# Performance work log

Measured on AMD Instinct MI355X. Metric: run time of the kernel, lower is better.

The kernel has to match this reference:

```python
import jax, jax.numpy as jnp
import numpy as np

N = 50000          # num nodes
DEG = 16           # fixed degree (uniform CSR)
E = N * DEG        # num edges
R = 8              # num relations
IN = 128
HID = 128
OUT = 40
BN_EPS = 1e-5


def setup_inputs() -> dict:
    key = jax.random.key(0)
    k = jax.random.split(key, 5)
    x = jax.random.normal(k[0], (N, IN), jnp.float32)
    # glorot-ish init for per-relation weights
    W1 = jax.random.normal(k[1], (R, IN, HID), jnp.float32) * (2.0 / (IN + HID)) ** 0.5
    W2 = jax.random.normal(k[2], (R, HID, OUT), jnp.float32) * (2.0 / (HID + OUT)) ** 0.5
    ptr = jnp.arange(N + 1, dtype=jnp.int32) * DEG            # CSR row offsets
    idx = jax.random.randint(k[3], (E,), 0, N, jnp.int32)     # neighbor (src) ids
    edge_types = jax.random.randint(k[4], (E,), 0, R, jnp.int32)
    return {
        "x": x, "W1": W1, "W2": W2,
        "bn_gamma": jnp.ones((HID,), jnp.float32),
        "bn_beta": jnp.zeros((HID,), jnp.float32),
        "bn_mean": jnp.zeros((HID,), jnp.float32),
        "bn_var": jnp.ones((HID,), jnp.float32),
        "ptr": ptr, "idx": idx, "edge_types": edge_types,
    }


def _rgcn_layer(h, W, ptr, idx, edge_types):
    # RGCNOP: out[i] = sum_{e in [ptr[i],ptr[i+1])} x[idx[e]] @ W[etype[e]]
    # Efficient form: transform every node by every relation once, then gather
    # the (src, etype) pair per edge and scatter-add into destinations.
    xr = jnp.einsum('nd,rdh->nrh', h, W)             # [N, R, H]
    msgs = xr[idx, edge_types]                       # [E, H] irregular gather
    deg = ptr[1:] - ptr[:-1]                         # [N]
    dst = jnp.repeat(jnp.arange(ptr.shape[0] - 1, dtype=jnp.int32), deg,
                     total_repeat_length=idx.shape[0])
    agg = jax.ops.segment_sum(msgs, dst, num_segments=ptr.shape[0] - 1)
    return agg / deg[:, None].astype(agg.dtype)      # degree normalization


def reference(x, W1, W2, bn_gamma, bn_beta, bn_mean, bn_var, ptr, idx, edge_types):
    h = _rgcn_layer(x, W1, ptr, idx, edge_types)
    # BatchNorm1d in eval mode (history_size=0, dropout inactive)
    h = (h - bn_mean) * jax.lax.rsqrt(bn_var + BN_EPS) * bn_gamma + bn_beta
    h = jax.nn.relu(h)
    h = _rgcn_layer(h, W2, ptr, idx, edge_types)
    return jax.nn.log_softmax(h, axis=-1)
```

## Files before the change

kernel.cpp:

```cpp
#include <hip/hip_runtime.h>
#include <math.h>

typedef __attribute__((ext_vector_type(8))) short bf16x8;
typedef __attribute__((ext_vector_type(4))) float f32x4;

constexpr int kN   = 50000;
constexpr int kIn  = 128;
constexpr int kHid = 128;
constexpr int kOut = 40;
constexpr int kNT  = 16;
constexpr int kLds = 1032;
constexpr float kBnEps = 1e-5f;

constexpr size_t kOffW2hi = 262144;
constexpr size_t kOffW2z  = 360448;
constexpr size_t kOffXb   = 524288;
constexpr size_t kOffBig  = 13324288;
constexpr size_t kZBytes  = (size_t)kN * 512 * 2;

__device__ inline float bf2f(ushort s) { return __uint_as_float(((uint)s) << 16); }

__device__ __forceinline__ ushort f2bf(float x) {
    uint u = __float_as_uint(x);
    u += 0x7FFFu + ((u >> 16) & 1u);
    return (ushort)(u >> 16);
}

__device__ __forceinline__ uint cvtpk(float a, float b) {
    uint r;
    asm("v_cvt_pk_bf16_f32 %0, %1, %2" : "=v"(r) : "v"(a), "v"(b));
    return r;
}

#define RD(V, J) __builtin_amdgcn_readlane((V), (J))

__device__ __forceinline__ void pack_unit(const float* __restrict__ W,
                                          ushort* __restrict__ dst,
                                          int N, int frag, int lane)
{
    const int kt = frag & 31;
    const int nt = frag >> 5;
    const int n  = nt * 16 + (lane & 15);
    const int q  = lane >> 4;
    float f[8];
    #pragma unroll
    for (int j = 0; j < 8; ++j) {
        const int k = kt * 32 + q * 8 + j;
        f[j] = (n < N) ? W[(size_t)k * N + n] : 0.f;
    }
    const size_t o = ((size_t)frag * 64 + lane) * 8;
    *(uint4*)&dst[o] = make_uint4(cvtpk(f[0], f[1]), cvtpk(f[2], f[3]),
                                  cvtpk(f[4], f[5]), cvtpk(f[6], f[7]));
}

__global__ __launch_bounds__(256)
void prep(const float* __restrict__ x,  ushort* __restrict__ xb,
          const float* __restrict__ W1, ushort* __restrict__ W1hi,
          const float* __restrict__ W2, ushort* __restrict__ W2hi,
          ushort* __restrict__ W2z, int useZ)
{
    const int b   = blockIdx.x;
    const int tid = threadIdx.x;
    if (b < 3125) {
        const size_t i = ((size_t)b * 256 + tid) * 8;
        const float4 v0 = *(const float4*)&x[i];
        const float4 v1 = *(const float4*)&x[i + 4];
        *(uint4*)&xb[i] = make_uint4(cvtpk(v0.x, v0.y), cvtpk(v0.z, v0.w),
                                     cvtpk(v1.x, v1.y), cvtpk(v1.z, v1.w));
    } else if (b < 3125 + 64) {
        pack_unit(W1, W1hi, kHid, (b - 3125) * 4 + (tid >> 6), tid & 63);
    } else if (b < 3213) {
        const int frag = (b - 3189) * 4 + (tid >> 6);
        if (frag < 96) pack_unit(W2, W2hi, kOut, frag, tid & 63);
    } else if (useZ) {
        const int frag = (b - 3213) * 4 + (tid >> 6);
        const int kt   = frag & 3;
        const int nt   = frag >> 2;
        const int lane = tid & 63;
        const int c    = nt * 16 + (lane & 15);
        const int r    = c >> 6;
        const int o    = c & 63;
        const int q    = lane >> 4;
        float f[8];
        #pragma unroll
        for (int j = 0; j < 8; ++j) {
            const int k = kt * 32 + q * 8 + j;
            f[j] = (o < kOut) ? W2[((size_t)r * kHid + k) * kOut + o] : 0.f;
        }
        const size_t of = ((size_t)frag * 64 + lane) * 8;
        *(uint4*)&W2z[of] = make_uint4(cvtpk(f[0], f[1]), cvtpk(f[2], f[3]),
                                       cvtpk(f[4], f[5]), cvtpk(f[6], f[7]));
    }
}

__device__ __forceinline__ void stage_fast(const char* fb, int vi, char* msW,
                                           int hOff, int lane)
{
    const int b = (lane & 7) * 16;
    #pragma unroll
    for (int u = 0; u < 4; ++u) {
        const int e   = u * 8 + (lane >> 3);
        const int src = __shfl(vi, e, 64);
        const uint4 v = *(const uint4*)(fb + (((size_t)(uint)src) << 8) + hOff + b);
        *(uint4*)(msW + e * 128 + (b ^ (u << 5))) = v;
    }
}

__device__ __forceinline__ void stage_slow(const char* fb,
                                           const int* __restrict__ idx,
                                           int p0, int p1, int deg0, int deg1,
                                           char* msW, int hOff, int lane)
{
    const int l31 = lane & 31;
    if (lane < 32) {
        for (int e = 0; e < 32; ++e) {
            const bool eok = (e < 16) ? (e < deg0) : ((e - 16) < deg1);
            uint val = 0;
            if (eok) {
                const int g = (e < 16) ? (p0 + e) : (p1 + (e - 16));
                const int s = idx[g];
                val = *(const uint*)(fb + (((size_t)(uint)s) << 8) + hOff + l31 * 4);
            }
            *(uint*)(msW + e * 128 + ((l31 * 4) ^ (((e >> 3) & 3) << 5))) = val;
        }
    }
}

__device__ __forceinline__ bf16x8 readB(const char* msW, int q, int m, int ntL)
{
    const char* ap = msW + q * 1024 + 2 * m + (((ntL ^ q) & 3) << 5);
    bf16x8 b;
    #pragma unroll
    for (int j = 0; j < 8; ++j) b[j] = *(const short*)(ap + j * 128);
    return b;
}

__device__ __forceinline__ void mfma_store(bf16x8 aS, bf16x8 bb, int fbase,
                                           int ntL, int w, int q, int m,
                                           ushort (*aggHi)[kLds])
{
    f32x4 z = {0.f, 0.f, 0.f, 0.f};
    const f32x4 d = __builtin_amdgcn_mfma_f32_16x16x32_bf16(aS, bb, z, 0, 0, 0);
    ushort* dst = &aggHi[2 * w + (q >> 1)][0];
    const int fcol = fbase + ntL * 16 + m;
    const int rb   = (q & 1) * 4;
    dst[(rb + 0) * 128 + fcol] = f2bf(d[0]);
    dst[(rb + 1) * 128 + fcol] = f2bf(d[1]);
    dst[(rb + 2) * 128 + fcol] = f2bf(d[2]);
    dst[(rb + 3) * 128 + fcol] = f2bf(d[3]);
}

__device__ __forceinline__ void phaseA_mfma(const ushort* __restrict__ feat,
                                            const int* __restrict__ ptr,
                                            const int* __restrict__ idx,
                                            const int* __restrict__ etype,
                                            int base, ushort (*aggHi)[kLds],
                                            char* msgs)
{
    const int lane = threadIdx.x & 63;
    const int w    = threadIdx.x >> 6;
    const int m    = lane & 15;
    const int q    = lane >> 4;
    const char* fb = (const char*)feat;

    const int node0 = base + 2 * w;
    const int p0 = ptr[node0];
    const int p1 = ptr[node0 + 1];
    const int p2 = ptr[node0 + 2];
    const int deg0 = p1 - p0, deg1 = p2 - p1;
    const bool fast = (deg0 == 16) && (deg1 == 16);

    const int vi = idx  [p0 + (lane & 31)];
    const int ve = etype[p0 + (lane & 31)];

    char* msW = msgs + w * 4096;

    int code;
    if (fast) {
        code = (((lane & 31) >> 4) << 3) | ve;
    } else {
        const int l31 = lane & 31;
        const bool eok = (l31 < 16) ? (l31 < deg0) : ((l31 - 16) < deg1);
        code = eok ? (((l31 >> 4) << 3) | ve) : 0xFF;
    }

    bf16x8 aS;
    #pragma unroll
    for (int j = 0; j < 8; ++j) {
        const int cj = __shfl(code, q * 8 + j, 64);
        aS[j] = (cj == m) ? (short)0x3F80 : (short)0;
    }

    if (fast) stage_fast(fb, vi, msW, 0, lane);
    else      stage_slow(fb, idx, p0, p1, deg0, deg1, msW, 0, lane);
    const bf16x8 b0 = readB(msW, q, m, 0);
    const bf16x8 b1 = readB(msW, q, m, 1);
    const bf16x8 b2 = readB(msW, q, m, 2);
    const bf16x8 b3 = readB(msW, q, m, 3);

    if (fast) stage_fast(fb, vi, msW, 128, lane);
    else      stage_slow(fb, idx, p0, p1, deg0, deg1, msW, 128, lane);

    mfma_store(aS, b0, 0, 0, w, q, m, aggHi);
    mfma_store(aS, b1, 0, 1, w, q, m, aggHi);
    mfma_store(aS, b2, 0, 2, w, q, m, aggHi);
    mfma_store(aS, b3, 0, 3, w, q, m, aggHi);

    const bf16x8 c0 = readB(msW, q, m, 0);
    const bf16x8 c1 = readB(msW, q, m, 1);
    const bf16x8 c2 = readB(msW, q, m, 2);
    const bf16x8 c3 = readB(msW, q, m, 3);
    mfma_store(aS, c0, 64, 0, w, q, m, aggHi);
    mfma_store(aS, c1, 64, 1, w, q, m, aggHi);
    mfma_store(aS, c2, 64, 2, w, q, m, aggHi);
    mfma_store(aS, c3, 64, 3, w, q, m, aggHi);
}

__global__ __launch_bounds__(512, 4)
void rgcn_layer1(const ushort* __restrict__ xb,
                 const ushort* __restrict__ W1hi,
                 const ushort* __restrict__ W2z,
                 const float* __restrict__ gamma, const float* __restrict__ beta,
                 const float* __restrict__ mean,  const float* __restrict__ var,
                 const int* __restrict__ ptr, const int* __restrict__ idx,
                 const int* __restrict__ etype,
                 ushort* __restrict__ big, int useZ)
{
    __shared__ ushort aggHi[kNT][kLds];
    __shared__ __align__(16) char msgs[8 * 4096];
    const int tid  = threadIdx.x;
    const int base = blockIdx.x * kNT;

    phaseA_mfma(xb, ptr, idx, etype, base, aggHi, msgs);
    __syncthreads();

    const int lane = tid & 63;
    const int wid  = tid >> 6;
    const int m    = lane & 15;
    const int q    = lane >> 4;

    const bf16x8* Bh = (const bf16x8*)W1hi + (size_t)wid * 32 * 64 + lane;
    f32x4 acc = {0.f, 0.f, 0.f, 0.f};

    #pragma unroll 4
    for (int kt = 0; kt < 32; ++kt) {
        const bf16x8 ah = *(const bf16x8*)&aggHi[m][kt * 32 + q * 8];
        const bf16x8 bh = Bh[(size_t)kt * 64];
        acc = __builtin_amdgcn_mfma_f32_16x16x32_bf16(ah, bh, acc, 0, 0, 0);
    }

    const int c = wid * 16 + m;
    const float g  = gamma[c] * rsqrtf(var[c] + kBnEps);
    const float mu = mean[c];
    const float bt = beta[c];
    float v[4];
    #pragma unroll
    for (int i = 0; i < 4; ++i) {
        const int node = base + q * 4 + i;
        const float invdeg = 1.0f / (float)(ptr[node + 1] - ptr[node]);
        v[i] = fmaxf((acc[i] * invdeg - mu) * g + bt, 0.f);
    }
    const uint p01 = cvtpk(v[0], v[1]);
    const uint p23 = cvtpk(v[2], v[3]);

    if (useZ) {
        ushort (*h1lds)[136] = (ushort (*)[136])(msgs + 16384);
        h1lds[q * 4 + 0][c] = (ushort)(p01 & 0xFFFFu);
        h1lds[q * 4 + 1][c] = (ushort)(p01 >> 16);
        h1lds[q * 4 + 2][c] = (ushort)(p23 & 0xFFFFu);
        h1lds[q * 4 + 3][c] = (ushort)(p23 >> 16);
        __syncthreads();

        ushort (*zlds)[512] = (ushort (*)[512])msgs;
        const bf16x8* B2 = (const bf16x8*)W2z;
        #pragma unroll
        for (int t = 0; t < 4; ++t) {
            const int nt = wid * 4 + t;
            f32x4 a2 = {0.f, 0.f, 0.f, 0.f};
            #pragma unroll
            for (int kt2 = 0; kt2 < 4; ++kt2) {
                const bf16x8 ah2 = *(const bf16x8*)&h1lds[m][kt2 * 32 + q * 8];
                const bf16x8 bh2 = B2[(size_t)(nt * 4 + kt2) * 64 + lane];
                a2 = __builtin_amdgcn_mfma_f32_16x16x32_bf16(ah2, bh2, a2, 0, 0, 0);
            }
            zlds[q * 4 + 0][nt * 16 + m] = f2bf(a2[0]);
            zlds[q * 4 + 1][nt * 16 + m] = f2bf(a2[1]);
            zlds[q * 4 + 2][nt * 16 + m] = f2bf(a2[2]);
            zlds[q * 4 + 3][nt * 16 + m] = f2bf(a2[3]);
        }
        __syncthreads();

        const int row = tid >> 5;
        const int cs  = (tid & 31) * 16;
        ushort* zp = big + ((size_t)(base + row)) * 512 + cs;
        *(uint4*)zp       = *(const uint4*)&zlds[row][cs];
        *(uint4*)(zp + 8) = *(const uint4*)&zlds[row][cs + 8];
    } else {
        const int n0 = base + q * 4;
        big[(size_t)(n0 + 0) * kHid + c] = (ushort)(p01 & 0xFFFFu);
        big[(size_t)(n0 + 1) * kHid + c] = (ushort)(p01 >> 16);
        big[(size_t)(n0 + 2) * kHid + c] = (ushort)(p23 & 0xFFFFu);
        big[(size_t)(n0 + 3) * kHid + c] = (ushort)(p23 >> 16);
    }
}

__global__ __launch_bounds__(512, 4)
void rgcn_layer2(const ushort* __restrict__ h1b,
                 const ushort* __restrict__ W2hi,
                 const int* __restrict__ ptr, const int* __restrict__ idx,
                 const int* __restrict__ etype,
                 float* __restrict__ out)
{
    __shared__ ushort aggHi[kNT][kLds];
    __shared__ __align__(16) char msgs[8 * 4096];
    __shared__ float logits[kNT][48];
    const int tid  = threadIdx.x;
    const int base = blockIdx.x * kNT;

    phaseA_mfma(h1b, ptr, idx, etype, base, aggHi, msgs);
    __syncthreads();

    const int lane = tid & 63;
    const int wid  = tid >> 6;
    const int m    = lane & 15;
    const int q    = lane >> 4;

    if (wid < 3) {
        const bf16x8* Bh = (const bf16x8*)W2hi + (size_t)wid * 32 * 64 + lane;
        f32x4 acc = {0.f, 0.f, 0.f, 0.f};
        #pragma unroll 4
        for (int kt = 0; kt < 32; ++kt) {
            const bf16x8 ah = *(const bf16x8*)&aggHi[m][kt * 32 + q * 8];
            const bf16x8 bh = Bh[(size_t)kt * 64];
            acc = __builtin_amdgcn_mfma_f32_16x16x32_bf16(ah, bh, acc, 0, 0, 0);
        }
        const int n = wid * 16 + m;
        if (n < kOut) {
            #pragma unroll
            for (int i = 0; i < 4; ++i) {
                const int node = base + q * 4 + i;
                const float invdeg = 1.0f / (float)(ptr[node + 1] - ptr[node]);
                logits[q * 4 + i][n] = acc[i] * invdeg;
            }
        }
    }
    __syncthreads();

    #pragma unroll
    for (int i = 0; i < 2; ++i) {
        const int nrow = wid * 2 + i;
        const int node = base + nrow;
        const float v = (lane < kOut) ? logits[nrow][lane] : -INFINITY;
        float mx = v;
        #pragma unroll
        for (int off = 32; off > 0; off >>= 1)
            mx = fmaxf(mx, __shfl_xor(mx, off, 64));
        float s = (lane < kOut) ? __expf(v - mx) : 0.f;
        #pragma unroll
        for (int off = 32; off > 0; off >>= 1)
            s += __shfl_xor(s, off, 64);
        if (lane < kOut)
            out[(size_t)node * kOut + lane] = v - mx - __logf(s);
    }
}

__global__ __launch_bounds__(256)
void rgcn_layer2z(const ushort* __restrict__ z,
                  const int* __restrict__ ptr, const int* __restrict__ idx,
                  const int* __restrict__ etype,
                  float* __restrict__ out)
{
    const int lane = threadIdx.x & 63;
    const int wv   = threadIdx.x >> 6;
    const int n0   = blockIdx.x * 16 + wv * 4;

    const int p0 = ptr[n0];
    const int d0 = ptr[n0 + 1] - p0;
    const int d1 = ptr[n0 + 2] - ptr[n0 + 1];
    const int d2 = ptr[n0 + 3] - ptr[n0 + 2];
    const int d3 = ptr[n0 + 4] - ptr[n0 + 3];
    const bool fast = (d0 == 16) & (d1 == 16) & (d2 == 16) & (d3 == 16);

    int vi = 0, ve = 0;
    if (fast) { vi = idx[p0 + lane]; ve = etype[p0 + lane]; }

    #pragma unroll
    for (int t = 0; t < 4; ++t) {
        const int node = n0 + t;
        float acc = 0.f;
        float invdeg;
        if (fast) {
            invdeg = 0.0625f;
            #pragma unroll
            for (int j = 0; j < 16; ++j) {
                const int e = t * 16 + j;
                const int s = RD(vi, e);
                const int r = RD(ve, e);
                acc += bf2f(z[(size_t)(uint)s * 512 + r * 64 + lane]);
            }
        } else {
            const int pa = ptr[node], pb = ptr[node + 1];
            invdeg = 1.0f / (float)(pb - pa);
            for (int e = pa; e < pb; ++e) {
                const int s = __builtin_amdgcn_readfirstlane(idx[e]);
                const int r = __builtin_amdgcn_readfirstlane(etype[e]);
                acc += bf2f(z[(size_t)(uint)s * 512 + r * 64 + lane]);
            }
        }
        const float v = (lane < kOut) ? acc * invdeg : -INFINITY;
        float mx = v;
        #pragma unroll
        for (int off = 32; off > 0; off >>= 1)
            mx = fmaxf(mx, __shfl_xor(mx, off, 64));
        float s2 = (lane < kOut) ? __expf(v - mx) : 0.f;
        #pragma unroll
        for (int off = 32; off > 0; off >>= 1)
            s2 += __shfl_xor(s2, off, 64);
        if (lane < kOut)
            out[(size_t)node * kOut + lane] = v - mx - __logf(s2);
    }
}

extern "C" void kernel_launch(void* const* d_in, const int* in_sizes, int n_in,
                              void* d_out, int out_size, void* d_ws, size_t ws_size,
                              hipStream_t stream)
{
    const float* x     = (const float*)d_in[0];
    const float* W1    = (const float*)d_in[1];
    const float* W2    = (const float*)d_in[2];
    const float* gamma = (const float*)d_in[3];
    const float* beta  = (const float*)d_in[4];
    const float* mean  = (const float*)d_in[5];
    const float* var   = (const float*)d_in[6];
    const int*   ptr   = (const int*)d_in[7];
    const int*   idx   = (const int*)d_in[8];
    const int*   et    = (const int*)d_in[9];
    float*       out   = (float*)d_out;

    char* ws = (char*)d_ws;
    ushort* W1hi = (ushort*)ws;
    ushort* W2hi = (ushort*)(ws + kOffW2hi);
    ushort* W2z  = (ushort*)(ws + kOffW2z);
    ushort* xb   = (ushort*)(ws + kOffXb);
    ushort* big  = (ushort*)(ws + kOffBig);

    const int useZ = (ws_size >= kOffBig + kZBytes) ? 1 : 0;

    prep<<<dim3(3245), dim3(256), 0, stream>>>(x, xb, W1, W1hi, W2, W2hi,
                                               W2z, useZ);

    dim3 grid(kN / kNT), block(512);
    rgcn_layer1<<<grid, block, 0, stream>>>(xb, W1hi, W2z, gamma, beta, mean,
                                            var, ptr, idx, et, big, useZ);
    if (useZ) {
        rgcn_layer2z<<<dim3(kN / 16), dim3(256), 0, stream>>>(big, ptr, idx,
                                                              et, out);
    } else {
        rgcn_layer2<<<grid, block, 0, stream>>>(big, W2hi, ptr, idx, et, out);
    }
}
```

Before: 184.9 us.

## Split layer-2 relation transform into separate zgemm kernel and use nontemporal stores

When the workspace is large enough, layer 1 now writes only the 128-wide h1 activations, and a new zgemm kernel computes the per-relation layer-2 transform into a separate buffer. This replaces the earlier fusion of that transform into layer 1. The intent is to lighten layer 1 (LDS pressure, extra syncs) at the cost of an extra launch and an extra h1 round trip through memory. Global outputs now use nontemporal stores to avoid polluting cache.

```diff
diff --git a/kernel.cpp b/kernel.cpp
--- a/kernel.cpp
+++ b/kernel.cpp
@@ -3,6 +3,7 @@
 
 typedef __attribute__((ext_vector_type(8))) short bf16x8;
 typedef __attribute__((ext_vector_type(4))) float f32x4;
+typedef __attribute__((ext_vector_type(4))) uint uint4v;
 
 constexpr int kN   = 50000;
 constexpr int kIn  = 128;
@@ -16,6 +17,7 @@
 constexpr size_t kOffW2z  = 360448;
 constexpr size_t kOffXb   = 524288;
 constexpr size_t kOffBig  = 13324288;
+constexpr size_t kH1Bytes = (size_t)kN * kHid * 2;
 constexpr size_t kZBytes  = (size_t)kN * 512 * 2;
 
 __device__ inline float bf2f(ushort s) { return __uint_as_float(((uint)s) << 16); }
@@ -33,6 +35,10 @@
 }
 
 #define RD(V, J) __builtin_amdgcn_readlane((V), (J))
+
+__device__ __forceinline__ void nt_store16(void* p, const void* src) {
+    __builtin_nontemporal_store(*(const uint4v*)src, (uint4v*)p);
+}
 
 __device__ __forceinline__ void pack_unit(const float* __restrict__ W,
                                           ushort* __restrict__ dst,
@@ -224,7 +230,7 @@
                  const float* __restrict__ mean,  const float* __restrict__ var,
                  const int* __restrict__ ptr, const int* __restrict__ idx,
                  const int* __restrict__ etype,
-                 ushort* __restrict__ big, int useZ)
+                 ushort* __restrict__ h1b, ushort* __restrict__ zbuf, int mode)
 {
     __shared__ ushort aggHi[kNT][kLds];
     __shared__ __align__(16) char msgs[8 * 4096];
@@ -263,7 +269,7 @@
     const uint p01 = cvtpk(v[0], v[1]);
     const uint p23 = cvtpk(v[2], v[3]);
 
-    if (useZ) {
+    if (mode == 1) {
         ushort (*h1lds)[136] = (ushort (*)[136])(msgs + 16384);
         h1lds[q * 4 + 0][c] = (ushort)(p01 & 0xFFFFu);
         h1lds[q * 4 + 1][c] = (ushort)(p01 >> 16);
@@ -292,16 +298,62 @@
 
         const int row = tid >> 5;
         const int cs  = (tid & 31) * 16;
-        ushort* zp = big + ((size_t)(base + row)) * 512 + cs;
-        *(uint4*)zp       = *(const uint4*)&zlds[row][cs];
-        *(uint4*)(zp + 8) = *(const uint4*)&zlds[row][cs + 8];
+        ushort* zp = zbuf + ((size_t)(base + row)) * 512 + cs;
+        nt_store16(zp,     &zlds[row][cs]);
+        nt_store16(zp + 8, &zlds[row][cs + 8]);
     } else {
         const int n0 = base + q * 4;
-        big[(size_t)(n0 + 0) * kHid + c] = (ushort)(p01 & 0xFFFFu);
-        big[(size_t)(n0 + 1) * kHid + c] = (ushort)(p01 >> 16);
-        big[(size_t)(n0 + 2) * kHid + c] = (ushort)(p23 & 0xFFFFu);
-        big[(size_t)(n0 + 3) * kHid + c] = (ushort)(p23 >> 16);
-    }
+        __builtin_nontemporal_store((ushort)(p01 & 0xFFFFu), &h1b[(size_t)(n0 + 0) * kHid + c]);
+        __builtin_nontemporal_store((ushort)(p01 >> 16),     &h1b[(size_t)(n0 + 1) * kHid + c]);
+        __builtin_nontemporal_store((ushort)(p23 & 0xFFFFu), &h1b[(size_t)(n0 + 2) * kHid + c]);
+        __builtin_nontemporal_store((ushort)(p23 >> 16),     &h1b[(size_t)(n0 + 3) * kHid + c]);
+    }
+}
+
+__global__ __launch_bounds__(512)
+void zgemm(const ushort* __restrict__ h1b, const ushort* __restrict__ W2z,
+           ushort* __restrict__ zbuf)
+{
+    __shared__ ushort h1lds[16][132];
+    __shared__ ushort zlds[16][520];
+    const int tid  = threadIdx.x;
+    const int base = blockIdx.x * 16;
+
+    {
+        const int r = tid >> 5;
+        const int cc = (tid & 31) * 4;
+        *(ushort4*)&h1lds[r][cc] = *(const ushort4*)&h1b[(size_t)(base + r) * kHid + cc];
+    }
+    __syncthreads();
+
+    const int lane = tid & 63;
+    const int wid  = tid >> 6;
+    const int m    = lane & 15;
+    const int q    = lane >> 4;
+    const bf16x8* B2 = (const bf16x8*)W2z;
+
+    #pragma unroll
+    for (int t = 0; t < 4; ++t) {
+        const int nt = wid * 4 + t;
+        f32x4 a2 = {0.f, 0.f, 0.f, 0.f};
+        #pragma unroll
+        for (int kt = 0; kt < 4; ++kt) {
+            const bf16x8 ah = *(const bf16x8*)&h1lds[m][kt * 32 + q * 8];
+            const bf16x8 bh = B2[(size_t)(nt * 4 + kt) * 64 + lane];
+            a2 = __builtin_amdgcn_mfma_f32_16x16x32_bf16(ah, bh, a2, 0, 0, 0);
+        }
+        zlds[q * 4 + 0][nt * 16 + m] = f2bf(a2[0]);
+        zlds[q * 4 + 1][nt * 16 + m] = f2bf(a2[1]);
+        zlds[q * 4 + 2][nt * 16 + m] = f2bf(a2[2]);
+        zlds[q * 4 + 3][nt * 16 + m] = f2bf(a2[3]);
+    }
+    __syncthreads();
+
+    const int row = tid >> 5;
+    const int cs  = (tid & 31) * 16;
+    ushort* zp = zbuf + ((size_t)(base + row)) * 512 + cs;
+    nt_store16(zp,     &zlds[row][cs]);
+    nt_store16(zp + 8, &zlds[row][cs + 8]);
 }
 
 __global__ __launch_bounds__(512, 4)
@@ -442,20 +494,37 @@
     ushort* W2hi = (ushort*)(ws + kOffW2hi);
     ushort* W2z  = (ushort*)(ws + kOffW2z);
     ushort* xb   = (ushort*)(ws + kOffXb);
-    ushort* big  = (ushort*)(ws + kOffBig);
-
-    const int useZ = (ws_size >= kOffBig + kZBytes) ? 1 : 0;
+
+    int mode;
+    ushort *h1b, *zbuf;
+    if (ws_size >= kOffBig + kH1Bytes + kZBytes) {
+        mode = 2;
+        h1b  = (ushort*)(ws + kOffBig);
+        zbuf = (ushort*)(ws + kOffBig + kH1Bytes);
+    } else if (ws_size >= kOffBig + kZBytes) {
+        mode = 1;
+        h1b  = (ushort*)(ws + kOffBig);
+        zbuf = (ushort*)(ws + kOffBig);
+    } else {
+        mode = 0;
+        h1b  = (ushort*)(ws + kOffBig);
+        zbuf = (ushort*)(ws + kOffBig);
+    }
 
     prep<<<dim3(3245), dim3(256), 0, stream>>>(x, xb, W1, W1hi, W2, W2hi,
-                                               W2z, useZ);
+                                               W2z, mode >= 1 ? 1 : 0);
 
     dim3 grid(kN / kNT), block(512);
     rgcn_layer1<<<grid, block, 0, stream>>>(xb, W1hi, W2z, gamma, beta, mean,
-                                            var, ptr, idx, et, big, useZ);
-    if (useZ) {
-        rgcn_layer2z<<<dim3(kN / 16), dim3(256), 0, stream>>>(big, ptr, idx,
+                                            var, ptr, idx, et, h1b, zbuf, mode);
+    if (mode == 2) {
+        zgemm<<<dim3(kN / 16), dim3(512), 0, stream>>>(h1b, W2z, zbuf);
+        rgcn_layer2z<<<dim3(kN / 16), dim3(256), 0, stream>>>(zbuf, ptr, idx,
+                                                              et, out);
+    } else if (mode == 1) {
+        rgcn_layer2z<<<dim3(kN / 16), dim3(256), 0, stream>>>(zbuf, ptr, idx,
                                                               et, out);
     } else {
-        rgcn_layer2<<<grid, block, 0, stream>>>(big, W2hi, ptr, idx, et, out);
-    }
-}
+        rgcn_layer2<<<grid, block, 0, stream>>>(h1b, W2hi, ptr, idx, et, out);
+    }
+}
```

After: 197.4 us. 1.07x slower.

## Compact per-relation Z buffer to 48 columns and split Z GEMM into separate kernel

Applied to the files above, without the earlier changes.

Shrinks the per-node transformed buffer from 8x64 to 8x48 bf16 columns so the layer-2 gather reads fewer bytes per edge. The second GEMM (h1 @ W2 for all relations) moves out of layer1 into a new zgemm kernel, so layer1 writes h1 to global memory and zgemm reads it back. The intent is to cut gather traffic and to lighten layer1's epilogue and LDS use. The cost is an extra kernel launch, an extra h1 round trip through global memory, a larger workspace requirement, and layer-2 rows that are no longer 512-byte aligned.

```diff
diff --git a/kernel.cpp b/kernel.cpp
--- a/kernel.cpp
+++ b/kernel.cpp
@@ -10,13 +10,15 @@
 constexpr int kOut = 40;
 constexpr int kNT  = 16;
 constexpr int kLds = 1032;
+constexpr int kZC  = 384;
 constexpr float kBnEps = 1e-5f;
 
 constexpr size_t kOffW2hi = 262144;
 constexpr size_t kOffW2z  = 360448;
 constexpr size_t kOffXb   = 524288;
 constexpr size_t kOffBig  = 13324288;
-constexpr size_t kZBytes  = (size_t)kN * 512 * 2;
+constexpr size_t kH1Bytes = (size_t)kN * kHid * 2;
+constexpr size_t kZBytes  = (size_t)kN * kZC * 2;
 
 __device__ inline float bf2f(ushort s) { return __uint_as_float(((uint)s) << 16); }
 
@@ -74,22 +76,24 @@
         if (frag < 96) pack_unit(W2, W2hi, kOut, frag, tid & 63);
     } else if (useZ) {
         const int frag = (b - 3213) * 4 + (tid >> 6);
-        const int kt   = frag & 3;
-        const int nt   = frag >> 2;
-        const int lane = tid & 63;
-        const int c    = nt * 16 + (lane & 15);
-        const int r    = c >> 6;
-        const int o    = c & 63;
-        const int q    = lane >> 4;
-        float f[8];
-        #pragma unroll
-        for (int j = 0; j < 8; ++j) {
-            const int k = kt * 32 + q * 8 + j;
-            f[j] = (o < kOut) ? W2[((size_t)r * kHid + k) * kOut + o] : 0.f;
-        }
-        const size_t of = ((size_t)frag * 64 + lane) * 8;
-        *(uint4*)&W2z[of] = make_uint4(cvtpk(f[0], f[1]), cvtpk(f[2], f[3]),
-                                       cvtpk(f[4], f[5]), cvtpk(f[6], f[7]));
+        if (frag < 96) {
+            const int kt   = frag & 3;
+            const int nt   = frag >> 2;
+            const int lane = tid & 63;
+            const int c    = nt * 16 + (lane & 15);
+            const int r    = c / 48;
+            const int o    = c % 48;
+            const int q    = lane >> 4;
+            float f[8];
+            #pragma unroll
+            for (int j = 0; j < 8; ++j) {
+                const int k = kt * 32 + q * 8 + j;
+                f[j] = (o < kOut) ? W2[((size_t)r * kHid + k) * kOut + o] : 0.f;
+            }
+            const size_t of = ((size_t)frag * 64 + lane) * 8;
+            *(uint4*)&W2z[of] = make_uint4(cvtpk(f[0], f[1]), cvtpk(f[2], f[3]),
+                                           cvtpk(f[4], f[5]), cvtpk(f[6], f[7]));
+        }
     }
 }
 
@@ -219,12 +223,11 @@
 __global__ __launch_bounds__(512, 4)
 void rgcn_layer1(const ushort* __restrict__ xb,
                  const ushort* __restrict__ W1hi,
-                 const ushort* __restrict__ W2z,
                  const float* __restrict__ gamma, const float* __restrict__ beta,
                  const float* __restrict__ mean,  const float* __restrict__ var,
                  const int* __restrict__ ptr, const int* __restrict__ idx,
                  const int* __restrict__ etype,
-                 ushort* __restrict__ big, int useZ)
+                 ushort* __restrict__ h1b)
 {
     __shared__ ushort aggHi[kNT][kLds];
     __shared__ __align__(16) char msgs[8 * 4096];
@@ -262,45 +265,57 @@
     }
     const uint p01 = cvtpk(v[0], v[1]);
     const uint p23 = cvtpk(v[2], v[3]);
-
-    if (useZ) {
-        ushort (*h1lds)[136] = (ushort (*)[136])(msgs + 16384);
-        h1lds[q * 4 + 0][c] = (ushort)(p01 & 0xFFFFu);
-        h1lds[q * 4 + 1][c] = (ushort)(p01 >> 16);
-        h1lds[q * 4 + 2][c] = (ushort)(p23 & 0xFFFFu);
-        h1lds[q * 4 + 3][c] = (ushort)(p23 >> 16);
-        __syncthreads();
-
-        ushort (*zlds)[512] = (ushort (*)[512])msgs;
-        const bf16x8* B2 = (const bf16x8*)W2z;
+    const int n0 = base + q * 4;
+    h1b[(size_t)(n0 + 0) * kHid + c] = (ushort)(p01 & 0xFFFFu);
+    h1b[(size_t)(n0 + 1) * kHid + c] = (ushort)(p01 >> 16);
+    h1b[(size_t)(n0 + 2) * kHid + c] = (ushort)(p23 & 0xFFFFu);
+    h1b[(size_t)(n0 + 3) * kHid + c] = (ushort)(p23 >> 16);
+}
+
+__global__ __launch_bounds__(512)
+void zgemm(const ushort* __restrict__ h1b, const ushort* __restrict__ W2z,
+           ushort* __restrict__ zbuf)
+{
+    __shared__ ushort h1lds[16][132];
+    __shared__ ushort zlds[16][392];
+    const int tid  = threadIdx.x;
+    const int base = blockIdx.x * 16;
+
+    {
+        const int r = tid >> 5;
+        const int cc = (tid & 31) * 4;
+        *(ushort4*)&h1lds[r][cc] = *(const ushort4*)&h1b[(size_t)(base + r) * kHid + cc];
+    }
+    __syncthreads();
+
+    const int lane = tid & 63;
+    const int wid  = tid >> 6;
+    const int m    = lane & 15;
+    const int q    = lane >> 4;
+    const bf16x8* B2 = (const bf16x8*)W2z;
+
+    #pragma unroll
+    for (int t = 0; t < 3; ++t) {
+        const int nt = wid * 3 + t;
+        f32x4 a2 = {0.f, 0.f, 0.f, 0.f};
         #pragma unroll
-        for (int t = 0; t < 4; ++t) {
-            const int nt = wid * 4 + t;
-            f32x4 a2 = {0.f, 0.f, 0.f, 0.f};
-            #pragma unroll
-            for (int kt2 = 0; kt2 < 4; ++kt2) {
-                const bf16x8 ah2 = *(const bf16x8*)&h1lds[m][kt2 * 32 + q * 8];
-                const bf16x8 bh2 = B2[(size_t)(nt * 4 + kt2) * 64 + lane];
-                a2 = __builtin_amdgcn_mfma_f32_16x16x32_bf16(ah2, bh2, a2, 0, 0, 0);
-            }
-            zlds[q * 4 + 0][nt * 16 + m] = f2bf(a2[0]);
-            zlds[q * 4 + 1][nt * 16 + m] = f2bf(a2[1]);
-            zlds[q * 4 + 2][nt * 16 + m] = f2bf(a2[2]);
-            zlds[q * 4 + 3][nt * 16 + m] = f2bf(a2[3]);
-        }
-        __syncthreads();
-
-        const int row = tid >> 5;
-        const int cs  = (tid & 31) * 16;
-        ushort* zp = big + ((size_t)(base + row)) * 512 + cs;
-        *(uint4*)zp       = *(const uint4*)&zlds[row][cs];
-        *(uint4*)(zp + 8) = *(const uint4*)&zlds[row][cs + 8];
-    } else {
-        const int n0 = base + q * 4;
-        big[(size_t)(n0 + 0) * kHid + c] = (ushort)(p01 & 0xFFFFu);
-        big[(size_t)(n0 + 1) * kHid + c] = (ushort)(p01 >> 16);
-        big[(size_t)(n0 + 2) * kHid + c] = (ushort)(p23 & 0xFFFFu);
-        big[(size_t)(n0 + 3) * kHid + c] = (ushort)(p23 >> 16);
+        for (int kt = 0; kt < 4; ++kt) {
+            const bf16x8 ah = *(const bf16x8*)&h1lds[m][kt * 32 + q * 8];
+            const bf16x8 bh = B2[(size_t)(nt * 4 + kt) * 64 + lane];
+            a2 = __builtin_amdgcn_mfma_f32_16x16x32_bf16(ah, bh, a2, 0, 0, 0);
+        }
+        zlds[q * 4 + 0][nt * 16 + m] = f2bf(a2[0]);
+        zlds[q * 4 + 1][nt * 16 + m] = f2bf(a2[1]);
+        zlds[q * 4 + 2][nt * 16 + m] = f2bf(a2[2]);
+        zlds[q * 4 + 3][nt * 16 + m] = f2bf(a2[3]);
+    }
+    __syncthreads();
+
+    for (int ch = tid; ch < 768; ch += 512) {
+        const int row = ch / 48;
+        const int off = (ch % 48) * 8;
+        *(uint4*)&zbuf[(size_t)(base + row) * kZC + off] =
+            *(const uint4*)&zlds[row][off];
     }
 }
 
@@ -396,7 +411,8 @@
                 const int e = t * 16 + j;
                 const int s = RD(vi, e);
                 const int r = RD(ve, e);
-                acc += bf2f(z[(size_t)(uint)s * 512 + r * 64 + lane]);
+                if (lane < 48)
+                    acc += bf2f(z[(size_t)(uint)s * kZC + r * 48 + lane]);
             }
         } else {
             const int pa = ptr[node], pb = ptr[node + 1];
@@ -404,7 +420,8 @@
             for (int e = pa; e < pb; ++e) {
                 const int s = __builtin_amdgcn_readfirstlane(idx[e]);
                 const int r = __builtin_amdgcn_readfirstlane(etype[e]);
-                acc += bf2f(z[(size_t)(uint)s * 512 + r * 64 + lane]);
+                if (lane < 48)
+                    acc += bf2f(z[(size_t)(uint)s * kZC + r * 48 + lane]);
             }
         }
         const float v = (lane < kOut) ? acc * invdeg : -INFINITY;
@@ -442,20 +459,22 @@
     ushort* W2hi = (ushort*)(ws + kOffW2hi);
     ushort* W2z  = (ushort*)(ws + kOffW2z);
     ushort* xb   = (ushort*)(ws + kOffXb);
-    ushort* big  = (ushort*)(ws + kOffBig);
-
-    const int useZ = (ws_size >= kOffBig + kZBytes) ? 1 : 0;
-
-    prep<<<dim3(3245), dim3(256), 0, stream>>>(x, xb, W1, W1hi, W2, W2hi,
-                                               W2z, useZ);
+    ushort* h1b  = (ushort*)(ws + kOffBig);
+    ushort* zbuf = (ushort*)(ws + kOffBig + kH1Bytes);
+
+    const int mode = (ws_size >= kOffBig + kH1Bytes + kZBytes) ? 2 : 0;
+
+    prep<<<dim3(3237), dim3(256), 0, stream>>>(x, xb, W1, W1hi, W2, W2hi,
+                                               W2z, mode == 2 ? 1 : 0);
 
     dim3 grid(kN / kNT), block(512);
-    rgcn_layer1<<<grid, block, 0, stream>>>(xb, W1hi, W2z, gamma, beta, mean,
-                                            var, ptr, idx, et, big, useZ);
-    if (useZ) {
-        rgcn_layer2z<<<dim3(kN / 16), dim3(256), 0, stream>>>(big, ptr, idx,
+    rgcn_layer1<<<grid, block, 0, stream>>>(xb, W1hi, gamma, beta, mean, var,
+                                            ptr, idx, et, h1b);
+    if (mode == 2) {
+        zgemm<<<dim3(kN / 16), dim3(512), 0, stream>>>(h1b, W2z, zbuf);
+        rgcn_layer2z<<<dim3(kN / 16), dim3(256), 0, stream>>>(zbuf, ptr, idx,
                                                               et, out);
     } else {
-        rgcn_layer2<<<grid, block, 0, stream>>>(big, W2hi, ptr, idx, et, out);
-    }
-}
+        rgcn_layer2<<<grid, block, 0, stream>>>(h1b, W2hi, ptr, idx, et, out);
+    }
+}
```

Result: slower. 215.2 us (+16.4%).
